# Optimization experiments

Hardware: AMD Instinct MI355X
Metric: run time of the kernel (lower is better)

## Reference

```python
import jax, jax.numpy as jnp
import numpy as np

B, S, D, H, F = 16, 577, 1024, 16, 4096
DH = D // H  # 64
EPS = 1e-6


def _layernorm(x, g, b):
    mu = jnp.mean(x, axis=-1, keepdims=True)
    var = jnp.mean(jnp.square(x - mu), axis=-1, keepdims=True)
    return (x - mu) * jax.lax.rsqrt(var + EPS) * g + b


def setup_inputs() -> dict:
    key = jax.random.key(0)
    ks = jax.random.split(key, 8)
    s = 1.0 / np.sqrt(D)
    sf = 1.0 / np.sqrt(F)
    return {
        "x": jax.random.normal(ks[0], (B, S, D), jnp.float32),
        "ln1_g": jnp.ones((D,), jnp.float32),
        "ln1_b": jnp.zeros((D,), jnp.float32),
        "wq": jax.random.normal(ks[1], (D, D), jnp.float32) * s,
        "bq": jnp.zeros((D,), jnp.float32),
        "wk": jax.random.normal(ks[2], (D, D), jnp.float32) * s,
        "bk": jnp.zeros((D,), jnp.float32),
        "wv": jax.random.normal(ks[3], (D, D), jnp.float32) * s,
        "bv": jnp.zeros((D,), jnp.float32),
        "wo": jax.random.normal(ks[4], (D, D), jnp.float32) * s,
        "bo": jnp.zeros((D,), jnp.float32),
        "ln2_g": jnp.ones((D,), jnp.float32),
        "ln2_b": jnp.zeros((D,), jnp.float32),
        "w1": jax.random.normal(ks[5], (D, F), jnp.float32) * s,
        "b1": jnp.zeros((F,), jnp.float32),
        "w2": jax.random.normal(ks[6], (F, D), jnp.float32) * sf,
        "b2": jnp.zeros((D,), jnp.float32),
    }


def reference(x, ln1_g, ln1_b, wq, bq, wk, bk, wv, bv, wo, bo,
              ln2_g, ln2_b, w1, b1, w2, b2):
    # --- attention sublayer ---
    h = x
    xn = _layernorm(x, ln1_g, ln1_b)
    q = (xn @ wq + bq).reshape(B, S, H, DH).transpose(0, 2, 1, 3)  # b h s d
    k = (xn @ wk + bk).reshape(B, S, H, DH).transpose(0, 2, 1, 3)
    v = (xn @ wv + bv).reshape(B, S, H, DH).transpose(0, 2, 1, 3)
    scores = jnp.einsum('bhqd,bhkd->bhqk', q, k) / np.sqrt(DH)
    probs = jax.nn.softmax(scores, axis=-1)
    ctx = jnp.einsum('bhqk,bhkd->bhqd', probs, v)
    ctx = ctx.transpose(0, 2, 1, 3).reshape(B, S, D)
    attn_out = ctx @ wo + bo  # dropout rate 0 -> mask of ones
    x = attn_out + h
    # --- MLP sublayer ---
    h = x
    xn = _layernorm(x, ln2_g, ln2_b)
    hmid = jax.nn.gelu(xn @ w1 + b1, approximate=False)
    x = (hmid @ w2 + b2) + h
    return x
```

## Files before the change

### kernel.cpp

```cpp
#include <hip/hip_runtime.h>
#include <hip/hip_fp16.h>
#include <math.h>

#define Bn 16
#define Sn 577
#define Dn 1024
#define Hn 16
#define DHn 64
#define Fn 4096
#define NROW (Bn*Sn)
#define EPSf 1e-6f

typedef unsigned short u16;
typedef unsigned int u32;
typedef __attribute__((ext_vector_type(8))) _Float16 f16x8;
typedef __attribute__((ext_vector_type(4))) float f32x4;

__device__ inline u16 f2h(float x) { return __half_as_ushort(__float2half(x)); }

__device__ inline void xcd_swizzle(int& bx, int& by) {
    int gx = gridDim.x;
    int nwg = gx * gridDim.y;
    int n = by * gx + bx;
    if ((nwg & 7) == 0) {
        int cpx = nwg >> 3;
        int w = (n & 7) * cpx + (n >> 3);
        bx = w % gx;
        by = w / gx;
    }
}

__device__ inline void conv_tile(const float* __restrict__ W, u16* __restrict__ T16,
                                 int K, int N, int bx, int by) {
    __shared__ float t[32][33];
    int n0 = bx * 32, k0 = by * 32;
    int tx = threadIdx.x & 31, ty = threadIdx.x >> 5;
#pragma unroll
    for (int i = 0; i < 4; i++) {
        int kk = ty * 4 + i;
        t[kk][tx] = W[(size_t)(k0 + kk) * N + n0 + tx];
    }
    __syncthreads();
#pragma unroll
    for (int i = 0; i < 4; i++) {
        int nn = ty * 4 + i;
        T16[(size_t)(n0 + nn) * K + k0 + tx] = f2h(t[tx][nn]);
    }
}

__device__ inline void ln_row_f16(const float* __restrict__ x,
                                  const float* __restrict__ g,
                                  const float* __restrict__ b,
                                  u16* __restrict__ oh, int row) {
    int tid = threadIdx.x;
    const float* xr = x + (size_t)row * Dn;
    float v[4];
    float s = 0.f;
#pragma unroll
    for (int i = 0; i < 4; i++) { v[i] = xr[tid + i * 256]; s += v[i]; }
    __shared__ float red[256];
    red[tid] = s; __syncthreads();
    for (int o = 128; o > 0; o >>= 1) { if (tid < o) red[tid] += red[tid + o]; __syncthreads(); }
    float mean = red[0] * (1.f / Dn);
    __syncthreads();
    float sq = 0.f;
#pragma unroll
    for (int i = 0; i < 4; i++) { float d = v[i] - mean; sq += d * d; }
    red[tid] = sq; __syncthreads();
    for (int o = 128; o > 0; o >>= 1) { if (tid < o) red[tid] += red[tid + o]; __syncthreads(); }
    float rstd = rsqrtf(red[0] * (1.f / Dn) + EPSf);
#pragma unroll
    for (int i = 0; i < 4; i++) {
        int c = tid + i * 256;
        float y = (v[i] - mean) * rstd * g[c] + b[c];
        oh[(size_t)row * Dn + c] = f2h(y);
    }
}

__global__ __launch_bounds__(256) void prep_all(
    const float* __restrict__ wq, const float* __restrict__ wk,
    const float* __restrict__ wv, const float* __restrict__ wo,
    const float* __restrict__ w1, const float* __restrict__ w2,
    const float* __restrict__ x, const float* __restrict__ ln1g,
    const float* __restrict__ ln1b,
    u16* __restrict__ wqkvT, u16* __restrict__ woT,
    u16* __restrict__ w1T, u16* __restrict__ w2T,
    u16* __restrict__ vtb, u16* __restrict__ xn_h)
{
    int t = blockIdx.x;
    if (t < 4096) {
        int which = t >> 10;
        int t2 = t & 1023;
        int bx = t2 & 31, by = t2 >> 5;
        const float* src = (which == 0) ? wq : (which == 1) ? wk : (which == 2) ? wv : wo;
        u16* dst = (which == 3) ? woT : (wqkvT + (size_t)which * 1024 * 1024);
        conv_tile(src, dst, 1024, 1024, bx, by);
    } else if (t < 8192) {
        int t2 = t - 4096;
        conv_tile(w1, w1T, 1024, 4096, t2 & 127, t2 >> 7);
    } else if (t < 12288) {
        int t2 = t - 8192;
        conv_tile(w2, w2T, 4096, 1024, t2 & 31, t2 >> 5);
    } else if (t < 13568) {
        size_t base = (size_t)(t - 12288) * 16384 + (size_t)threadIdx.x * 16;
        char* p = (char*)vtb + base;
        float4 z = make_float4(0.f, 0.f, 0.f, 0.f);
#pragma unroll
        for (int i = 0; i < 4; i++) *(float4*)(p + (size_t)i * 4096) = z;
    } else {
        ln_row_f16(x, ln1g, ln1b, xn_h, t - 13568);
    }
}

__global__ __launch_bounds__(256) void ln_f16(const float* __restrict__ x,
                                              const float* __restrict__ g,
                                              const float* __restrict__ b,
                                              u16* __restrict__ oh) {
    ln_row_f16(x, g, b, oh, blockIdx.x);
}

__global__ __launch_bounds__(256) void ln_kernel(const float* __restrict__ x,
                                                 const float* __restrict__ g,
                                                 const float* __restrict__ b,
                                                 float* __restrict__ out) {
    int row = blockIdx.x;
    int tid = threadIdx.x;
    const float* xr = x + (size_t)row * Dn;
    float v[4];
    float s = 0.f;
#pragma unroll
    for (int i = 0; i < 4; i++) { v[i] = xr[tid + i * 256]; s += v[i]; }
    __shared__ float red[256];
    red[tid] = s; __syncthreads();
    for (int o = 128; o > 0; o >>= 1) { if (tid < o) red[tid] += red[tid + o]; __syncthreads(); }
    float mean = red[0] * (1.f / Dn);
    __syncthreads();
    float sq = 0.f;
#pragma unroll
    for (int i = 0; i < 4; i++) { float d = v[i] - mean; sq += d * d; }
    red[tid] = sq; __syncthreads();
    for (int o = 128; o > 0; o >>= 1) { if (tid < o) red[tid] += red[tid + o]; __syncthreads(); }
    float rstd = rsqrtf(red[0] * (1.f / Dn) + EPSf);
    float* orow = out + (size_t)row * Dn;
#pragma unroll
    for (int i = 0; i < 4; i++) {
        int c = tid + i * 256;
        orow[c] = (v[i] - mean) * rstd * g[c] + b[c];
    }
}

__device__ inline void gld_lds16(const u16* g, u16* l) {
    __builtin_amdgcn_global_load_lds((const __attribute__((address_space(1))) void*)g,
                                     (__attribute__((address_space(3))) void*)l,
                                     16, 0, 0);
}

template<int EPI>
__global__ __launch_bounds__(256, 4) void gemm_1t(
    const u16* __restrict__ A, const u16* __restrict__ B,
    const float* __restrict__ bias, const float* __restrict__ resid,
    float* __restrict__ Cf, u16* __restrict__ Ch,
    int M, int N, int K)
{
    __shared__ u16 lds[2][2][4096];
    const int tid = threadIdx.x;
    const int l = tid & 63, w = tid >> 6;
    const int wr = (w >> 1) * 64, wc = (w & 1) * 64;
    int bx = blockIdx.x, by = blockIdx.y;
    xcd_swizzle(bx, by);
    const int row0 = by * 128, col0 = bx * 128;

    const int sg = w * 2;
    const int tl0 = sg * 16 + (l >> 2);
    const int tl1 = tl0 + 16;
    const int kq0 = (l & 3) ^ ((tl0 >> 1) & 3);
    const int kq1 = (l & 3) ^ ((tl1 >> 1) & 3);
    int ga0 = row0 + tl0; if (ga0 > M - 1) ga0 = M - 1;
    int ga1 = row0 + tl1; if (ga1 > M - 1) ga1 = M - 1;
    int gb0 = col0 + tl0; if (gb0 > N - 1) gb0 = N - 1;
    int gb1 = col0 + tl1; if (gb1 > N - 1) gb1 = N - 1;
    const u16* pA0 = A + (size_t)ga0 * K + kq0 * 8;
    const u16* pA1 = A + (size_t)ga1 * K + kq1 * 8;
    const u16* pB0 = B + (size_t)gb0 * K + kq0 * 8;
    const u16* pB1 = B + (size_t)gb1 * K + kq1 * 8;

    int offA[4], offB[4];
#pragma unroll
    for (int i = 0; i < 4; i++) {
        int ra = wr + i * 16 + (l & 15);
        offA[i] = ra * 32 + (((l >> 4) ^ ((ra >> 1) & 3)) << 3);
        int rb = wc + i * 16 + (l & 15);
        offB[i] = rb * 32 + (((l >> 4) ^ ((rb >> 1) & 3)) << 3);
    }

    f32x4 acc[4][4];
#pragma unroll
    for (int i = 0; i < 4; i++)
#pragma unroll
        for (int j = 0; j < 4; j++)
            acc[i][j] = (f32x4){0.f, 0.f, 0.f, 0.f};

    auto STAGE = [&](int buf, int kk) {
        gld_lds16(pA0 + kk, &lds[buf][0][(sg + 0) * 512]);
        gld_lds16(pA1 + kk, &lds[buf][0][(sg + 1) * 512]);
        gld_lds16(pB0 + kk, &lds[buf][1][(sg + 0) * 512]);
        gld_lds16(pB1 + kk, &lds[buf][1][(sg + 1) * 512]);
    };
    auto COMPUTE = [&](int buf) {
        f16x8 af[4], bf4[4];
#pragma unroll
        for (int i = 0; i < 4; i++) af[i] = *(const f16x8*)(&lds[buf][0][offA[i]]);
#pragma unroll
        for (int j = 0; j < 4; j++) bf4[j] = *(const f16x8*)(&lds[buf][1][offB[j]]);
#pragma unroll
        for (int i = 0; i < 4; i++)
#pragma unroll
            for (int j = 0; j < 4; j++)
                acc[i][j] = __builtin_amdgcn_mfma_f32_16x16x32_f16(af[i], bf4[j], acc[i][j], 0, 0, 0);
    };

    const int nk = K / 32;
    STAGE(0, 0);
    __syncthreads();
    for (int t = 0; t < nk; t += 2) {
        if (t + 1 < nk) STAGE(1, (t + 1) * 32);
        COMPUTE(0);
        __syncthreads();
        if (t + 2 < nk) STAGE(0, (t + 2) * 32);
        COMPUTE(1);
        __syncthreads();
    }

    const int rq = l >> 4;
#pragma unroll
    for (int i = 0; i < 4; i++) {
#pragma unroll
        for (int j = 0; j < 4; j++) {
            int col = col0 + wc + j * 16 + (l & 15);
            float bs = bias[col];
#pragma unroll
            for (int r = 0; r < 4; r++) {
                int rowg = row0 + wr + i * 16 + rq * 4 + r;
                if (rowg >= M) continue;
                float vv = acc[i][j][r] + bs;
                size_t o = (size_t)rowg * N + col;
                if (EPI == 1) {
                    float gl = 0.5f * vv * (1.f + erff(vv * 0.70710678118654752f));
                    Ch[o] = f2h(gl);
                } else if (EPI == 2) {
                    Cf[o] = vv + resid[o];
                } else {
                    Cf[o] = vv;
                }
            }
        }
    }
}

template<int EPI>
__global__ __launch_bounds__(512, 4) void gemm_256(
    const u16* __restrict__ A, const u16* __restrict__ B,
    const float* __restrict__ bias, const float* __restrict__ resid,
    float* __restrict__ Cf, u16* __restrict__ Ch,
    int M, int N, int K)
{
    __shared__ u16 ldsA[2][256 * 32];
    __shared__ u16 ldsB[2][128 * 32];
    const int tid = threadIdx.x;
    const int l = tid & 63, w = tid >> 6;
    const int wr = (w >> 1) * 64, wc = (w & 1) * 64;
    int bx = blockIdx.x, by = blockIdx.y;
    xcd_swizzle(bx, by);
    const int row0 = by * 256, col0 = bx * 128;

    const int sgA = w * 2;
    const int tlA0 = sgA * 16 + (l >> 2);
    const int tlA1 = tlA0 + 16;
    const int kqA0 = (l & 3) ^ ((tlA0 >> 1) & 3);
    const int kqA1 = (l & 3) ^ ((tlA1 >> 1) & 3);
    int gaA0 = row0 + tlA0; if (gaA0 > M - 1) gaA0 = M - 1;
    int gaA1 = row0 + tlA1; if (gaA1 > M - 1) gaA1 = M - 1;
    const u16* pA0 = A + (size_t)gaA0 * K + kqA0 * 8;
    const u16* pA1 = A + (size_t)gaA1 * K + kqA1 * 8;
    const int tlB = w * 16 + (l >> 2);
    const int kqB = (l & 3) ^ ((tlB >> 1) & 3);
    int gbB = col0 + tlB; if (gbB > N - 1) gbB = N - 1;
    const u16* pB = B + (size_t)gbB * K + kqB * 8;

    int offA[4], offB[4];
#pragma unroll
    for (int i = 0; i < 4; i++) {
        int ra = wr + i * 16 + (l & 15);
        offA[i] = ra * 32 + (((l >> 4) ^ ((ra >> 1) & 3)) << 3);
        int rb = wc + i * 16 + (l & 15);
        offB[i] = rb * 32 + (((l >> 4) ^ ((rb >> 1) & 3)) << 3);
    }

    f32x4 acc[4][4];
#pragma unroll
    for (int i = 0; i < 4; i++)
#pragma unroll
        for (int j = 0; j < 4; j++)
            acc[i][j] = (f32x4){0.f, 0.f, 0.f, 0.f};

    auto STAGE = [&](int buf, int kk) {
        gld_lds16(pA0 + kk, &ldsA[buf][(sgA + 0) * 512]);
        gld_lds16(pA1 + kk, &ldsA[buf][(sgA + 1) * 512]);
        gld_lds16(pB + kk, &ldsB[buf][w * 512]);
    };
    auto COMPUTE = [&](int buf) {
        f16x8 af[4], bf4[4];
#pragma unroll
        for (int i = 0; i < 4; i++) af[i] = *(const f16x8*)(&ldsA[buf][offA[i]]);
#pragma unroll
        for (int j = 0; j < 4; j++) bf4[j] = *(const f16x8*)(&ldsB[buf][offB[j]]);
#pragma unroll
        for (int i = 0; i < 4; i++)
#pragma unroll
            for (int j = 0; j < 4; j++)
                acc[i][j] = __builtin_amdgcn_mfma_f32_16x16x32_f16(af[i], bf4[j], acc[i][j], 0, 0, 0);
    };

    const int nk = K / 32;
    STAGE(0, 0);
    __syncthreads();
    for (int t = 0; t < nk; t += 2) {
        if (t + 1 < nk) STAGE(1, (t + 1) * 32);
        COMPUTE(0);
        __syncthreads();
        if (t + 2 < nk) STAGE(0, (t + 2) * 32);
        COMPUTE(1);
        __syncthreads();
    }

    const int rq = l >> 4;
#pragma unroll
    for (int i = 0; i < 4; i++) {
#pragma unroll
        for (int j = 0; j < 4; j++) {
            int col = col0 + wc + j * 16 + (l & 15);
            float bs = bias[col];
#pragma unroll
            for (int r = 0; r < 4; r++) {
                int rowg = row0 + wr + i * 16 + rq * 4 + r;
                if (rowg >= M) continue;
                float vv = acc[i][j][r] + bs;
                size_t o = (size_t)rowg * N + col;
                if (EPI == 1) {
                    float gl = 0.5f * vv * (1.f + erff(vv * 0.70710678118654752f));
                    Ch[o] = f2h(gl);
                } else if (EPI == 2) {
                    Cf[o] = vv + resid[o];
                } else {
                    Cf[o] = vv;
                }
            }
        }
    }
}

__global__ __launch_bounds__(256, 4) void gemm_qkv(
    const u16* __restrict__ A, const u16* __restrict__ B,
    const float* __restrict__ bq, const float* __restrict__ bk,
    const float* __restrict__ bv,
    u16* __restrict__ qb, u16* __restrict__ kb, u16* __restrict__ vt,
    int M, int N, int K)
{
    __shared__ u16 lds[2][2][4096];
    const int tid = threadIdx.x;
    const int l = tid & 63, w = tid >> 6;
    const int wr = (w >> 1) * 64, wc = (w & 1) * 64;
    int bx = blockIdx.x, by = blockIdx.y;
    xcd_swizzle(bx, by);
    const int row0 = by * 128, col0 = bx * 128;

    const int sg = w * 2;
    const int tl0 = sg * 16 + (l >> 2);
    const int tl1 = tl0 + 16;
    const int kq0 = (l & 3) ^ ((tl0 >> 1) & 3);
    const int kq1 = (l & 3) ^ ((tl1 >> 1) & 3);
    int ga0 = row0 + tl0; if (ga0 > M - 1) ga0 = M - 1;
    int ga1 = row0 + tl1; if (ga1 > M - 1) ga1 = M - 1;
    int gb0 = col0 + tl0; if (gb0 > N - 1) gb0 = N - 1;
    int gb1 = col0 + tl1; if (gb1 > N - 1) gb1 = N - 1;
    const u16* pA0 = A + (size_t)ga0 * K + kq0 * 8;
    const u16* pA1 = A + (size_t)ga1 * K + kq1 * 8;
    const u16* pB0 = B + (size_t)gb0 * K + kq0 * 8;
    const u16* pB1 = B + (size_t)gb1 * K + kq1 * 8;

    int offA[4], offB[4];
#pragma unroll
    for (int i = 0; i < 4; i++) {
        int ra = wr + i * 16 + (l & 15);
        offA[i] = ra * 32 + (((l >> 4) ^ ((ra >> 1) & 3)) << 3);
        int rb = wc + i * 16 + (l & 15);
        offB[i] = rb * 32 + (((l >> 4) ^ ((rb >> 1) & 3)) << 3);
    }

    f32x4 acc[4][4];
#pragma unroll
    for (int i = 0; i < 4; i++)
#pragma unroll
        for (int j = 0; j < 4; j++)
            acc[i][j] = (f32x4){0.f, 0.f, 0.f, 0.f};

    auto STAGE = [&](int buf, int kk) {
        gld_lds16(pA0 + kk, &lds[buf][0][(sg + 0) * 512]);
        gld_lds16(pA1 + kk, &lds[buf][0][(sg + 1) * 512]);
        gld_lds16(pB0 + kk, &lds[buf][1][(sg + 0) * 512]);
        gld_lds16(pB1 + kk, &lds[buf][1][(sg + 1) * 512]);
    };
    auto COMPUTE = [&](int buf) {
        f16x8 af[4], bf4[4];
#pragma unroll
        for (int i = 0; i < 4; i++) af[i] = *(const f16x8*)(&lds[buf][0][offA[i]]);
#pragma unroll
        for (int j = 0; j < 4; j++) bf4[j] = *(const f16x8*)(&lds[buf][1][offB[j]]);
#pragma unroll
        for (int i = 0; i < 4; i++)
#pragma unroll
            for (int j = 0; j < 4; j++)
                acc[i][j] = __builtin_amdgcn_mfma_f32_16x16x32_f16(af[i], bf4[j], acc[i][j], 0, 0, 0);
    };

    const int nk = K / 32;
    STAGE(0, 0);
    __syncthreads();
    for (int t = 0; t < nk; t += 2) {
        if (t + 1 < nk) STAGE(1, (t + 1) * 32);
        COMPUTE(0);
        __syncthreads();
        if (t + 2 < nk) STAGE(0, (t + 2) * 32);
        COMPUTE(1);
        __syncthreads();
    }

    const int rq = l >> 4;
#pragma unroll
    for (int i = 0; i < 4; i++) {
#pragma unroll
        for (int j = 0; j < 4; j++) {
            int col = col0 + wc + j * 16 + (l & 15);
#pragma unroll
            for (int r = 0; r < 4; r++) {
                int rowg = row0 + wr + i * 16 + rq * 4 + r;
                if (rowg >= M) continue;
                float a = acc[i][j][r];
                if (col < 1024) {
                    qb[(size_t)rowg * 1024 + col] = f2h((a + bq[col]) * 0.125f);
                } else if (col < 2048) {
                    int c2 = col - 1024;
                    kb[(size_t)rowg * 1024 + c2] = f2h(a + bk[c2]);
                } else {
                    int c2 = col - 2048;
                    u32 rg = (u32)rowg;
                    u32 bb = rg / 577u;
                    u32 key = rg - bb * 577u;
                    vt[((size_t)((bb * 16 + (c2 >> 6)) * 64 + (c2 & 63))) * 640 + key] =
                        f2h(a + bv[c2]);
                }
            }
        }
    }
}

__global__ __launch_bounds__(256) void flash_mfma(const u16* __restrict__ Qg,
                                                  const u16* __restrict__ Kg,
                                                  const u16* __restrict__ Vt,
                                                  u16* __restrict__ Oh) {
    __shared__ u16 Kl[64 * 64];
    __shared__ u16 Vl[64 * 64];
    __shared__ u16 Pl[64][72];

    int bx = blockIdx.x, by = blockIdx.y;
    xcd_swizzle(bx, by);
    const int qt = bx, bh = by;
    const int b = bh >> 4, h = bh & 15;
    const int tid = threadIdx.x;
    const int l = tid & 63, w = tid >> 6;
    const int q0 = qt * 64;

    int qrow = q0 + w * 16 + (l & 15); if (qrow > 576) qrow = 576;
    const u16* qp = Qg + ((size_t)(b * 577 + qrow)) * 1024 + h * 64 + (l >> 4) * 8;
    f16x8 qf0 = *(const f16x8*)qp;
    f16x8 qf1 = *(const f16x8*)(qp + 32);

    const int swk = ((l & 7) ^ (l >> 3)) * 8;

    f32x4 ctx[4];
#pragma unroll
    for (int d = 0; d < 4; d++) ctx[d] = (f32x4){0.f, 0.f, 0.f, 0.f};
    float m_r[4], l_r[4];
#pragma unroll
    for (int r = 0; r < 4; r++) { m_r[r] = -1e30f; l_r[r] = 0.f; }

#pragma unroll
    for (int c2 = 0; c2 < 2; ++c2) {
        int c = w * 2 + c2;
        int key = c * 8 + (l >> 3); if (key > 576) key = 576;
        const u16* ksrc = Kg + ((size_t)(b * 577 + key)) * 1024 + h * 64 + swk;
        gld_lds16(ksrc, Kl + c * 512);
        int d = c * 8 + (l >> 3);
        const u16* vsrc = Vt + ((size_t)(bh * 64 + d)) * 640 + swk;
        gld_lds16(vsrc, Vl + c * 512);
    }
    __syncthreads();

    for (int kt = 0; kt < 10; ++kt) {
        f16x8 kreg[2], vreg[2];
        if (kt < 9) {
            const int kb2 = (kt + 1) * 64;
#pragma unroll
            for (int c2 = 0; c2 < 2; ++c2) {
                int c = w * 2 + c2;
                int key = kb2 + c * 8 + (l >> 3); if (key > 576) key = 576;
                kreg[c2] = *(const f16x8*)(Kg + ((size_t)(b * 577 + key)) * 1024 + h * 64 + swk);
                int d = c * 8 + (l >> 3);
                vreg[c2] = *(const f16x8*)(Vt + ((size_t)(bh * 64 + d)) * 640 + kb2 + swk);
            }
        }

        const int kb = kt * 64;
        f32x4 sc[4];
#pragma unroll
        for (int sub = 0; sub < 4; ++sub) {
            sc[sub] = (f32x4){0.f, 0.f, 0.f, 0.f};
            int rr = sub * 16 + (l & 15);
            int c0 = (l >> 4) ^ (rr & 7);
            int c1 = ((l >> 4) + 4) ^ (rr & 7);
            f16x8 kf0 = *(const f16x8*)(Kl + rr * 64 + c0 * 8);
            f16x8 kf1 = *(const f16x8*)(Kl + rr * 64 + c1 * 8);
            sc[sub] = __builtin_amdgcn_mfma_f32_16x16x32_f16(qf0, kf0, sc[sub], 0, 0, 0);
            sc[sub] = __builtin_amdgcn_mfma_f32_16x16x32_f16(qf1, kf1, sc[sub], 0, 0, 0);
        }

        bool valid[4];
#pragma unroll
        for (int sub = 0; sub < 4; ++sub) valid[sub] = (kb + sub * 16 + (l & 15)) < Sn;

#pragma unroll
        for (int r = 0; r < 4; ++r) {
            float s0 = valid[0] ? sc[0][r] : -1e30f;
            float s1 = valid[1] ? sc[1][r] : -1e30f;
            float s2 = valid[2] ? sc[2][r] : -1e30f;
            float s3 = valid[3] ? sc[3][r] : -1e30f;
            float mx = fmaxf(fmaxf(s0, s1), fmaxf(s2, s3));
            mx = fmaxf(mx, __shfl_xor(mx, 1));
            mx = fmaxf(mx, __shfl_xor(mx, 2));
            mx = fmaxf(mx, __shfl_xor(mx, 4));
            mx = fmaxf(mx, __shfl_xor(mx, 8));
            float mnew = fmaxf(m_r[r], mx);
            float scale = __expf(m_r[r] - mnew);
            float p0 = valid[0] ? __expf(s0 - mnew) : 0.f;
            float p1 = valid[1] ? __expf(s1 - mnew) : 0.f;
            float p2 = valid[2] ? __expf(s2 - mnew) : 0.f;
            float p3 = valid[3] ? __expf(s3 - mnew) : 0.f;
            int prow = w * 16 + (l >> 4) * 4 + r;
            int pcol = l & 15;
            Pl[prow][pcol]      = f2h(p0);
            Pl[prow][pcol + 16] = f2h(p1);
            Pl[prow][pcol + 32] = f2h(p2);
            Pl[prow][pcol + 48] = f2h(p3);
            float rsum = p0 + p1 + p2 + p3;
            rsum += __shfl_xor(rsum, 1);
            rsum += __shfl_xor(rsum, 2);
            rsum += __shfl_xor(rsum, 4);
            rsum += __shfl_xor(rsum, 8);
            l_r[r] = l_r[r] * scale + rsum;
            m_r[r] = mnew;
#pragma unroll
            for (int d = 0; d < 4; ++d) ctx[d][r] *= scale;
        }

#pragma unroll
        for (int ks = 0; ks < 2; ++ks) {
            f16x8 pf = *(const f16x8*)(&Pl[w * 16 + (l & 15)][ks * 32 + (l >> 4) * 8]);
#pragma unroll
            for (int d = 0; d < 4; ++d) {
                int rr = d * 16 + (l & 15);
                int cv = (ks * 4 + (l >> 4)) ^ (rr & 7);
                f16x8 vf = *(const f16x8*)(Vl + rr * 64 + cv * 8);
                ctx[d] = __builtin_amdgcn_mfma_f32_16x16x32_f16(pf, vf, ctx[d], 0, 0, 0);
            }
        }
        __syncthreads();

        if (kt < 9) {
#pragma unroll
            for (int c2 = 0; c2 < 2; ++c2) {
                int c = w * 2 + c2;
                *(f16x8*)(Kl + c * 512 + l * 8) = kreg[c2];
                *(f16x8*)(Vl + c * 512 + l * 8) = vreg[c2];
            }
            __syncthreads();
        }
    }

#pragma unroll
    for (int r = 0; r < 4; ++r) {
        int q = q0 + w * 16 + (l >> 4) * 4 + r;
        if (q >= Sn) continue;
        float inv = 1.f / l_r[r];
#pragma unroll
        for (int d = 0; d < 4; ++d) {
            float t = ctx[d][r] * inv;
            size_t o = ((size_t)(b * 577 + q)) * 1024 + h * 64 + d * 16 + (l & 15);
            Oh[o] = f2h(t);
        }
    }
}

template<int EPI>
__global__ __launch_bounds__(256) void gemm_kernel(const float* __restrict__ A,
                                                   const float* __restrict__ W,
                                                   const float* __restrict__ bias,
                                                   const float* __restrict__ resid,
                                                   float* __restrict__ C,
                                                   int M, int N, int K) {
    const int BM = 64, BN = 64, BK = 16;
    __shared__ float As[BK][BM + 1];
    __shared__ float Ws[BK][BN];
    int tx = threadIdx.x, ty = threadIdx.y;
    int tid = ty * 16 + tx;
    int row0 = blockIdx.y * BM, col0 = blockIdx.x * BN;
    float acc[4][4] = {};
    for (int k0 = 0; k0 < K; k0 += BK) {
#pragma unroll
        for (int i = 0; i < 4; i++) {
            int idx = i * 256 + tid;
            int ar = idx >> 4, ac = idx & 15;
            int grow = row0 + ar;
            As[ac][ar] = (grow < M) ? A[(size_t)grow * K + k0 + ac] : 0.f;
        }
#pragma unroll
        for (int i = 0; i < 4; i++) {
            int idx = i * 256 + tid;
            int wr = idx >> 6, wcc = idx & 63;
            Ws[wr][wcc] = W[(size_t)(k0 + wr) * N + col0 + wcc];
        }
        __syncthreads();
#pragma unroll
        for (int kk = 0; kk < BK; kk++) {
            float a[4], wv[4];
#pragma unroll
            for (int i = 0; i < 4; i++) a[i] = As[kk][ty * 4 + i];
#pragma unroll
            for (int j = 0; j < 4; j++) wv[j] = Ws[kk][tx * 4 + j];
#pragma unroll
            for (int i = 0; i < 4; i++)
#pragma unroll
                for (int j = 0; j < 4; j++)
                    acc[i][j] += a[i] * wv[j];
        }
        __syncthreads();
    }
#pragma unroll
    for (int i = 0; i < 4; i++) {
        int grow = row0 + ty * 4 + i;
        if (grow >= M) continue;
#pragma unroll
        for (int j = 0; j < 4; j++) {
            int gcol = col0 + tx * 4 + j;
            float r = acc[i][j] + bias[gcol];
            if (EPI == 1) r = 0.5f * r * (1.f + erff(r * 0.70710678118654752f));
            if (EPI == 2) r += resid[(size_t)grow * N + gcol];
            C[(size_t)grow * N + gcol] = r;
        }
    }
}

__global__ __launch_bounds__(256) void flash_kernel(const float* __restrict__ Q,
                                                    const float* __restrict__ K,
                                                    const float* __restrict__ V,
                                                    float* __restrict__ Of) {
    __shared__ float Qs[64][68];
    __shared__ float KT[64][68];
    __shared__ float Vs[64][68];
    __shared__ float Ps[64][68];

    int qt = blockIdx.x;
    int bh = blockIdx.y;
    int b = bh >> 4, h = bh & 15;
    int tid = threadIdx.x;
    int tx = tid & 15, ty = tid >> 4;
    size_t base = ((size_t)b * Sn) * Dn + (size_t)h * DHn;
    int q0 = qt * 64;

    {
        int r = tid >> 4;
        int c = (tid & 15) * 4;
#pragma unroll
        for (int i = 0; i < 4; i++) {
            int rr = r + i * 16;
            int gq = q0 + rr;
            float4 val = make_float4(0.f, 0.f, 0.f, 0.f);
            if (gq < Sn) val = *(const float4*)&Q[base + (size_t)gq * Dn + c];
            Qs[rr][c + 0] = val.x * 0.125f;
            Qs[rr][c + 1] = val.y * 0.125f;
            Qs[rr][c + 2] = val.z * 0.125f;
            Qs[rr][c + 3] = val.w * 0.125f;
        }
    }

    float m_r[4], l_r[4], acc[4][4];
#pragma unroll
    for (int i = 0; i < 4; i++) {
        m_r[i] = -1e30f; l_r[i] = 0.f;
#pragma unroll
        for (int j = 0; j < 4; j++) acc[i][j] = 0.f;
    }

    for (int kt = 0; kt < 10; kt++) {
        int kb = kt * 64;
        {
            int r = tid >> 4;
            int c = (tid & 15) * 4;
#pragma unroll
            for (int i = 0; i < 4; i++) {
                int rr = r + i * 16;
                int gk = kb + rr;
                float4 kv = make_float4(0.f, 0.f, 0.f, 0.f);
                float4 vv = make_float4(0.f, 0.f, 0.f, 0.f);
                if (gk < Sn) {
                    kv = *(const float4*)&K[base + (size_t)gk * Dn + c];
                    vv = *(const float4*)&V[base + (size_t)gk * Dn + c];
                }
                KT[c + 0][rr] = kv.x;
                KT[c + 1][rr] = kv.y;
                KT[c + 2][rr] = kv.z;
                KT[c + 3][rr] = kv.w;
                Vs[rr][c + 0] = vv.x;
                Vs[rr][c + 1] = vv.y;
                Vs[rr][c + 2] = vv.z;
                Vs[rr][c + 3] = vv.w;
            }
        }
        __syncthreads();

        float s[4][4] = {};
#pragma unroll
        for (int kk4 = 0; kk4 < 16; kk4++) {
            float4 a4[4], b4[4];
#pragma unroll
            for (int i = 0; i < 4; i++) a4[i] = *(const float4*)&Qs[ty * 4 + i][kk4 * 4];
#pragma unroll
            for (int q = 0; q < 4; q++) b4[q] = *(const float4*)&KT[kk4 * 4 + q][tx * 4];
#pragma unroll
            for (int i = 0; i < 4; i++) {
                float av[4] = {a4[i].x, a4[i].y, a4[i].z, a4[i].w};
#pragma unroll
                for (int q = 0; q < 4; q++) {
                    s[i][0] += av[q] * b4[q].x;
                    s[i][1] += av[q] * b4[q].y;
                    s[i][2] += av[q] * b4[q].z;
                    s[i][3] += av[q] * b4[q].w;
                }
            }
        }

        bool cvalid[4];
#pragma unroll
        for (int j = 0; j < 4; j++) cvalid[j] = (kb + tx * 4 + j) < Sn;
#pragma unroll
        for (int i = 0; i < 4; i++) {
            float lmax = -1e30f;
#pragma unroll
            for (int j = 0; j < 4; j++) if (cvalid[j]) lmax = fmaxf(lmax, s[i][j]);
            lmax = fmaxf(lmax, __shfl_xor(lmax, 1));
            lmax = fmaxf(lmax, __shfl_xor(lmax, 2));
            lmax = fmaxf(lmax, __shfl_xor(lmax, 4));
            lmax = fmaxf(lmax, __shfl_xor(lmax, 8));
            float mnew = fmaxf(m_r[i], lmax);
            float scale = __expf(m_r[i] - mnew);
            float rsum = 0.f;
#pragma unroll
            for (int j = 0; j < 4; j++) {
                float p = cvalid[j] ? __expf(s[i][j] - mnew) : 0.f;
                s[i][j] = p;
                rsum += p;
            }
            rsum += __shfl_xor(rsum, 1);
            rsum += __shfl_xor(rsum, 2);
            rsum += __shfl_xor(rsum, 4);
            rsum += __shfl_xor(rsum, 8);
            l_r[i] = l_r[i] * scale + rsum;
            m_r[i] = mnew;
#pragma unroll
            for (int j = 0; j < 4; j++) acc[i][j] *= scale;
        }

#pragma unroll
        for (int i = 0; i < 4; i++)
#pragma unroll
            for (int j = 0; j < 4; j++)
                Ps[ty * 4 + i][tx * 4 + j] = s[i][j];
        __syncthreads();

#pragma unroll
        for (int kk4 = 0; kk4 < 16; kk4++) {
            float4 a4[4], b4[4];
#pragma unroll
            for (int i = 0; i < 4; i++) a4[i] = *(const float4*)&Ps[ty * 4 + i][kk4 * 4];
#pragma unroll
            for (int q = 0; q < 4; q++) b4[q] = *(const float4*)&Vs[kk4 * 4 + q][tx * 4];
#pragma unroll
            for (int i = 0; i < 4; i++) {
                float av[4] = {a4[i].x, a4[i].y, a4[i].z, a4[i].w};
#pragma unroll
                for (int q = 0; q < 4; q++) {
                    acc[i][0] += av[q] * b4[q].x;
                    acc[i][1] += av[q] * b4[q].y;
                    acc[i][2] += av[q] * b4[q].z;
                    acc[i][3] += av[q] * b4[q].w;
                }
            }
        }
        __syncthreads();
    }

#pragma unroll
    for (int i = 0; i < 4; i++) {
        int gq = q0 + ty * 4 + i;
        if (gq >= Sn) continue;
        float inv = 1.f / l_r[i];
#pragma unroll
        for (int j = 0; j < 4; j++)
            Of[base + (size_t)gq * Dn + tx * 4 + j] = acc[i][j] * inv;
    }
}

extern "C" void kernel_launch(void* const* d_in, const int* in_sizes, int n_in,
                              void* d_out, int out_size, void* d_ws, size_t ws_size,
                              hipStream_t stream) {
    const float* x    = (const float*)d_in[0];
    const float* ln1g = (const float*)d_in[1];
    const float* ln1b = (const float*)d_in[2];
    const float* wq   = (const float*)d_in[3];
    const float* bq   = (const float*)d_in[4];
    const float* wk   = (const float*)d_in[5];
    const float* bk   = (const float*)d_in[6];
    const float* wv   = (const float*)d_in[7];
    const float* bv   = (const float*)d_in[8];
    const float* wo   = (const float*)d_in[9];
    const float* bo   = (const float*)d_in[10];
    const float* ln2g = (const float*)d_in[11];
    const float* ln2b = (const float*)d_in[12];
    const float* w1   = (const float*)d_in[13];
    const float* b1   = (const float*)d_in[14];
    const float* w2   = (const float*)d_in[15];
    const float* b2   = (const float*)d_in[16];
    float* out = (float*)d_out;
    char* ws = (char*)d_ws;

    const size_t WHALF_D = (size_t)1024 * 1024 * 2;
    const size_t WHALF_F = (size_t)4096 * 1024 * 2;
    const size_t HALF_XN = (size_t)NROW * 1024 * 2;
    const size_t BASE_A  = 8 * WHALF_D + 4 * WHALF_F;
    const size_t NEED = BASE_A + 10 * HALF_XN;

    if (ws_size >= NEED) {
        u16* wqkvT = (u16*)(ws);
        u16* woT   = (u16*)(ws + 6 * WHALF_D);
        u16* w1T   = (u16*)(ws + 8 * WHALF_D);
        u16* w2T   = (u16*)(ws + 8 * WHALF_D + 2 * WHALF_F);
        char* S = ws + BASE_A;
        u16* xn_h  = (u16*)(S + 0 * HALF_XN);
        u16* qb    = (u16*)(S + 2 * HALF_XN);
        u16* kb2   = (u16*)(S + 3 * HALF_XN);
        u16* vtb   = (u16*)(S + 4 * HALF_XN);
        u16* ctx_h = (u16*)(S + 8 * HALF_XN);
        u16* xn2_h = (u16*)(S + 9 * HALF_XN);
        u16* hm_h  = (u16*)(S + 0 * HALF_XN);

        prep_all<<<22800, 256, 0, stream>>>(wq, wk, wv, wo, w1, w2,
                                            x, ln1g, ln1b,
                                            wqkvT, woT, w1T, w2T, vtb, xn_h);

        gemm_qkv<<<dim3(24, 73), 256, 0, stream>>>(xn_h, wqkvT, bq, bk, bv,
                                                   qb, kb2, vtb, NROW, 3072, 1024);
        flash_mfma<<<dim3(10, Bn * Hn), 256, 0, stream>>>(qb, kb2, vtb, ctx_h);
        gemm_1t<2><<<dim3(8, 73), 256, 0, stream>>>(
            ctx_h, woT, bo, x, out, nullptr, NROW, 1024, 1024);
        ln_f16<<<NROW, 256, 0, stream>>>(out, ln2g, ln2b, xn2_h);
        gemm_256<1><<<dim3(32, 37), 512, 0, stream>>>(
            xn2_h, w1T, b1, nullptr, nullptr, hm_h, NROW, 4096, 1024);
        gemm_1t<2><<<dim3(8, 73), 256, 0, stream>>>(
            hm_h, w2T, b2, out, out, nullptr, NROW, 1024, 4096);
    } else {
        const size_t SZ = (size_t)NROW * Dn * sizeof(float);
        float* qbuf  = (float*)(ws);
        float* kbuf  = (float*)(ws + SZ);
        float* vbuf  = (float*)(ws + 2 * SZ);
        float* hmid  = (float*)(ws);
        float* xnbuf = (float*)(ws + 4 * SZ);
        float* ctx   = (float*)(ws + 5 * SZ);
        float* x1    = (float*)(ws + 6 * SZ);
        dim3 blk2(16, 16);
        dim3 gD(Dn / 64, (NROW + 63) / 64);
        dim3 gF(Fn / 64, (NROW + 63) / 64);
        ln_kernel<<<NROW, 256, 0, stream>>>(x, ln1g, ln1b, xnbuf);
        gemm_kernel<0><<<gD, blk2, 0, stream>>>(xnbuf, wq, bq, nullptr, qbuf, NROW, Dn, Dn);
        gemm_kernel<0><<<gD, blk2, 0, stream>>>(xnbuf, wk, bk, nullptr, kbuf, NROW, Dn, Dn);
        gemm_kernel<0><<<gD, blk2, 0, stream>>>(xnbuf, wv, bv, nullptr, vbuf, NROW, Dn, Dn);
        flash_kernel<<<dim3(10, Bn * Hn), 256, 0, stream>>>(qbuf, kbuf, vbuf, ctx);
        gemm_kernel<2><<<gD, blk2, 0, stream>>>(ctx, wo, bo, x, x1, NROW, Dn, Dn);
        ln_kernel<<<NROW, 256, 0, stream>>>(x1, ln2g, ln2b, xnbuf);
        gemm_kernel<1><<<gF, blk2, 0, stream>>>(xnbuf, w1, b1, nullptr, hmid, NROW, Fn, Dn);
        gemm_kernel<2><<<gD, blk2, 0, stream>>>(hmid, w2, b2, x1, out, NROW, Dn, Fn);
    }
}
```

Measured before the change: 549.7 us.

## Add 256x256-tile 8-wave GEMM with ping-pong LDS schedule for FFN up-projection

Adds a gemm_8p kernel that computes 256x256 output tiles with 8 waves and 128 KB of dynamic LDS. Loads are spread across the four sub-steps of each k-iteration, with barriers and setprio interleaving MFMA and global-to-LDS loads. It replaces gemm_256 for the W1 GEMM with fused GELU, aiming for more data reuse per tile and better overlap of loads with compute. The cost is one block per CU occupancy, a hipFuncSetAttribute call on every launch, and a fallback path if the attribute call fails.

```diff
diff --git a/kernel.cpp b/kernel.cpp
--- a/kernel.cpp
+++ b/kernel.cpp
@@ -153,6 +153,154 @@
     __builtin_amdgcn_global_load_lds((const __attribute__((address_space(1))) void*)g,
                                      (__attribute__((address_space(3))) void*)l,
                                      16, 0, 0);
+}
+
+template<int EPI>
+__global__ __launch_bounds__(512, 2) void gemm_8p(
+    const u16* __restrict__ A, const u16* __restrict__ B,
+    const float* __restrict__ bias, const float* __restrict__ resid,
+    float* __restrict__ Cf, u16* __restrict__ Ch,
+    int M, int N, int K)
+{
+    extern __shared__ u16 dl[];
+    const int tid = threadIdx.x;
+    const int l = tid & 63, w = tid >> 6;
+    const int wr = (w >> 2) * 128, wc = (w & 3) * 64;
+    int bx = blockIdx.x, by = blockIdx.y;
+    xcd_swizzle(bx, by);
+    const int row0 = by * 256, col0 = bx * 256;
+
+    const int lr = l >> 3;
+    const int sw8 = ((l & 7) ^ lr) * 8;
+    const u16* pA[4];
+    const u16* pB[4];
+#pragma unroll
+    for (int g = 0; g < 4; g++) {
+        int ra = row0 + w * 8 + g * 64 + lr; if (ra > M - 1) ra = M - 1;
+        int rb = col0 + w * 8 + g * 64 + lr; if (rb > N - 1) rb = N - 1;
+        pA[g] = A + (size_t)ra * K + sw8;
+        pB[g] = B + (size_t)rb * K + sw8;
+    }
+
+    auto GLD_A = [&](int buf, int g, int kt) {
+        gld_lds16(pA[g] + kt * 64, dl + (size_t)buf * 32768 + (w * 8 + g * 64) * 64);
+    };
+    auto GLD_B = [&](int buf, int g, int kt) {
+        gld_lds16(pB[g] + kt * 64, dl + (size_t)buf * 32768 + 16384 + (w * 8 + g * 64) * 64);
+    };
+
+    const int c0 = (((l >> 4) + 0) ^ (l & 7)) * 8;
+    const int c1 = (((l >> 4) + 4) ^ (l & 7)) * 8;
+    int aoff[8], boff[4];
+#pragma unroll
+    for (int i = 0; i < 8; i++) aoff[i] = (wr + i * 16 + (l & 15)) * 64;
+#pragma unroll
+    for (int j = 0; j < 4; j++) boff[j] = 16384 + (wc + j * 16 + (l & 15)) * 64;
+
+    f32x4 acc[8][4];
+#pragma unroll
+    for (int i = 0; i < 8; i++)
+#pragma unroll
+        for (int j = 0; j < 4; j++)
+            acc[i][j] = (f32x4){0.f, 0.f, 0.f, 0.f};
+
+    const int nk = K / 64;
+
+#pragma unroll
+    for (int g = 0; g < 4; g++) GLD_A(0, g, 0);
+#pragma unroll
+    for (int g = 0; g < 4; g++) GLD_B(0, g, 0);
+#pragma unroll
+    for (int g = 0; g < 4; g++) GLD_B(1, g, 1);
+    GLD_A(1, 0, 1);
+    GLD_A(1, 2, 1);
+
+    f16x8 bf0[4], bf1[4];
+
+    for (int t = 0; t < nk; ++t) {
+        const int buf = t & 1;
+        const u16* P = dl + (size_t)buf * 32768;
+
+        if (t == nk - 1) asm volatile("s_waitcnt vmcnt(0)" ::: "memory");
+        else             asm volatile("s_waitcnt vmcnt(6)" ::: "memory");
+        __builtin_amdgcn_s_barrier();
+
+        {
+            f16x8 aA0 = *(const f16x8*)(P + aoff[0] + c0);
+            f16x8 aA1 = *(const f16x8*)(P + aoff[0] + c1);
+            f16x8 aB0 = *(const f16x8*)(P + aoff[1] + c0);
+            f16x8 aB1 = *(const f16x8*)(P + aoff[1] + c1);
+#pragma unroll
+            for (int j = 0; j < 4; j++) {
+                bf0[j] = *(const f16x8*)(P + boff[j] + c0);
+                bf1[j] = *(const f16x8*)(P + boff[j] + c1);
+            }
+            if (t + 1 < nk) {
+                GLD_A(buf ^ 1, 1, t + 1);
+                GLD_A(buf ^ 1, 3, t + 1);
+            }
+            __builtin_amdgcn_s_barrier();
+            __builtin_amdgcn_s_setprio(1);
+#pragma unroll
+            for (int j = 0; j < 4; j++) {
+                acc[0][j] = __builtin_amdgcn_mfma_f32_16x16x32_f16(aA0, bf0[j], acc[0][j], 0, 0, 0);
+                acc[0][j] = __builtin_amdgcn_mfma_f32_16x16x32_f16(aA1, bf1[j], acc[0][j], 0, 0, 0);
+                acc[1][j] = __builtin_amdgcn_mfma_f32_16x16x32_f16(aB0, bf0[j], acc[1][j], 0, 0, 0);
+                acc[1][j] = __builtin_amdgcn_mfma_f32_16x16x32_f16(aB1, bf1[j], acc[1][j], 0, 0, 0);
+            }
+            __builtin_amdgcn_s_setprio(0);
+            __builtin_amdgcn_s_barrier();
+        }
+
+#pragma unroll
+        for (int q = 1; q < 4; q++) {
+            f16x8 aA0 = *(const f16x8*)(P + aoff[2 * q] + c0);
+            f16x8 aA1 = *(const f16x8*)(P + aoff[2 * q] + c1);
+            f16x8 aB0 = *(const f16x8*)(P + aoff[2 * q + 1] + c0);
+            f16x8 aB1 = *(const f16x8*)(P + aoff[2 * q + 1] + c1);
+            if (t + 2 < nk) {
+                if (q == 1) { GLD_B(buf, 0, t + 2); GLD_B(buf, 1, t + 2); }
+                if (q == 2) { GLD_B(buf, 2, t + 2); GLD_B(buf, 3, t + 2); }
+                if (q == 3) { GLD_A(buf, 0, t + 2); GLD_A(buf, 2, t + 2); }
+            }
+            __builtin_amdgcn_s_barrier();
+            __builtin_amdgcn_s_setprio(1);
+#pragma unroll
+            for (int j = 0; j < 4; j++) {
+                acc[2 * q][j]     = __builtin_amdgcn_mfma_f32_16x16x32_f16(aA0, bf0[j], acc[2 * q][j], 0, 0, 0);
+                acc[2 * q][j]     = __builtin_amdgcn_mfma_f32_16x16x32_f16(aA1, bf1[j], acc[2 * q][j], 0, 0, 0);
+                acc[2 * q + 1][j] = __builtin_amdgcn_mfma_f32_16x16x32_f16(aB0, bf0[j], acc[2 * q + 1][j], 0, 0, 0);
+                acc[2 * q + 1][j] = __builtin_amdgcn_mfma_f32_16x16x32_f16(aB1, bf1[j], acc[2 * q + 1][j], 0, 0, 0);
+            }
+            __builtin_amdgcn_s_setprio(0);
+            __builtin_amdgcn_s_barrier();
+        }
+    }
+
+    const int rq = l >> 4;
+#pragma unroll
+    for (int i = 0; i < 8; i++) {
+#pragma unroll
+        for (int j = 0; j < 4; j++) {
+            int col = col0 + wc + j * 16 + (l & 15);
+            float bs = bias[col];
+#pragma unroll
+            for (int r = 0; r < 4; r++) {
+                int rowg = row0 + wr + i * 16 + rq * 4 + r;
+                if (rowg >= M) continue;
+                float vv = acc[i][j][r] + bs;
+                size_t o = (size_t)rowg * N + col;
+                if (EPI == 1) {
+                    float gl = 0.5f * vv * (1.f + erff(vv * 0.70710678118654752f));
+                    Ch[o] = f2h(gl);
+                } else if (EPI == 2) {
+                    Cf[o] = vv + resid[o];
+                } else {
+                    Cf[o] = vv;
+                }
+            }
+        }
+    }
 }
 
 template<int EPI>
@@ -882,8 +1030,18 @@
         gemm_1t<2><<<dim3(8, 73), 256, 0, stream>>>(
             ctx_h, woT, bo, x, out, nullptr, NROW, 1024, 1024);
         ln_f16<<<NROW, 256, 0, stream>>>(out, ln2g, ln2b, xn2_h);
-        gemm_256<1><<<dim3(32, 37), 512, 0, stream>>>(
-            xn2_h, w1T, b1, nullptr, nullptr, hm_h, NROW, 4096, 1024);
+
+        bool use8p = (hipFuncSetAttribute(
+                          reinterpret_cast<const void*>(&gemm_8p<1>),
+                          hipFuncAttributeMaxDynamicSharedMemorySize,
+                          131072) == hipSuccess);
+        if (use8p) {
+            gemm_8p<1><<<dim3(16, 37), 512, 131072, stream>>>(
+                xn2_h, w1T, b1, nullptr, nullptr, hm_h, NROW, 4096, 1024);
+        } else {
+            gemm_256<1><<<dim3(32, 37), 512, 0, stream>>>(
+                xn2_h, w1T, b1, nullptr, nullptr, hm_h, NROW, 4096, 1024);
+        }
         gemm_1t<2><<<dim3(8, 73), 256, 0, stream>>>(
             hm_h, w2T, b2, out, out, nullptr, NROW, 1024, 4096);
     } else {
```

Measured after the change: 618.0 us. 1.12x slower.
